# Kernel optimization log

Measured on AMD Instinct MI355X. Metric: run time of the kernel, lower is better.

The kernel has to match this reference:

```python
import jax, jax.numpy as jnp
import numpy as np
from jax import lax

N = 2048       # number of groups (rows of x)
T = 32768      # total tokens across all ragged segments
D_SEQ = 128    # per-token feature dim
D_LSTM = 512   # RNN hidden per direction (= min(512, d_hidden//2))
D_X = 512      # node feature dim (LazyLinear input)
D_HIDDEN = 2048
D_PROJ = D_HIDDEN - 2 * D_LSTM  # 1024


def setup_inputs() -> dict:
    key = jax.random.key(0)
    ks = jax.random.split(key, 12)
    x = jax.random.normal(ks[0], (N, D_X), jnp.float32)
    seqs = jax.random.normal(ks[1], (T, D_SEQ), jnp.float32)
    # sorted group ids; concat arange(N) to guarantee every group is present
    extra = jax.random.randint(ks[2], (T - N,), 0, N)
    masks = jnp.sort(jnp.concatenate([jnp.arange(N), extra]))
    s = 1.0 / np.sqrt(D_LSTM)
    u = lambda k, shape: jax.random.uniform(k, shape, jnp.float32, -s, s)
    return {
        "x": x, "seqs": seqs, "masks": masks,
        "W_ih_f": u(ks[3], (D_LSTM, D_SEQ)), "W_hh_f": u(ks[4], (D_LSTM, D_LSTM)), "b_f": u(ks[5], (D_LSTM,)),
        "W_ih_b": u(ks[6], (D_LSTM, D_SEQ)), "W_hh_b": u(ks[7], (D_LSTM, D_LSTM)), "b_b": u(ks[8], (D_LSTM,)),
        "Wx": u(ks[9], (D_PROJ, D_X)), "bx": u(ks[10], (D_PROJ,)),
    }


def _dir_scan(pre, starts, W_hh):
    # pre: [T, H] precomputed input projection (+bias); starts: [T] bool segment-start flags.
    # h_t = tanh(pre_t + W_hh h_{t-1}), with h reset to 0 at each segment start.
    def step(h, inp):
        p, st = inp
        h = jnp.tanh(p + jnp.where(st, 0.0, 1.0) * (h @ W_hh.T))
        return h, h
    h0 = jnp.zeros((pre.shape[1],), pre.dtype)
    _, hs = lax.scan(step, h0, (pre, starts))
    return hs  # [T, H]


def reference(x, seqs, masks, W_ih_f, W_hh_f, b_f, W_ih_b, W_hh_b, b_b, Wx, bx):
    # segment boundaries (masks is sorted -> contiguous segments)
    starts = jnp.concatenate([jnp.ones((1,), bool), masks[1:] != masks[:-1]])
    m_rev = masks[::-1]
    starts_rev = jnp.concatenate([jnp.ones((1,), bool), m_rev[1:] != m_rev[:-1]])

    # bidirectional tanh-RNN over each segment (single-layer, like nn.RNN)
    h_f = _dir_scan(seqs @ W_ih_f.T + b_f, starts, W_hh_f)                 # [T, 512]
    h_b = _dir_scan((seqs @ W_ih_b.T + b_b)[::-1], starts_rev, W_hh_b)[::-1]  # [T, 512]
    hidden = jnp.concatenate([h_f, h_b], axis=-1)                           # [T, 1024]

    # mean pool per segment -> one embedding per group
    counts = jax.ops.segment_sum(jnp.ones((masks.shape[0],), hidden.dtype), masks, num_segments=N)
    pooled = jax.ops.segment_sum(hidden, masks, num_segments=N) / counts[:, None]  # [N, 1024]

    # x projection then concat: [x_proj | pooled]
    return jnp.concatenate([x @ Wx.T + bx, pooled], axis=-1)  # [N, 2048]
```

## Files before the change

### kernel.cpp

```cpp
#include <hip/hip_runtime.h>
#include <cstdint>
#include <cstddef>

#define T_N    32768
#define N_SEG  2048
#define DSEQ   128
#define DLSTM  512
#define DX     512
#define DPROJ  1024
#define OUTW   2048
#define WSCALE 2873.6827f
#define SXQ    15.875f
#define LOG2E2 2.8853900817779268f
#define DEQH   (2.8853900817779268f/(2873.6827f*127.0f))
#define MAGICF 12582912.0f
#define MAGIC_C (12582912.0f + 127.0f)

typedef __attribute__((ext_vector_type(8))) short short8;
typedef __attribute__((ext_vector_type(4))) float f32x4;
typedef __attribute__((ext_vector_type(4))) int i32x4;

#if __has_builtin(__builtin_amdgcn_exp2f)
#define EXP2F(x) __builtin_amdgcn_exp2f(x)
#else
#define EXP2F(x) __expf((x) * 0.6931471805599453f)
#endif
#if __has_builtin(__builtin_amdgcn_rcpf)
#define RCPF(x) __builtin_amdgcn_rcpf(x)
#else
#define RCPF(x) (1.0f / (x))
#endif

#define PIN(x) asm volatile("" : "+v"(x))

__device__ inline unsigned int cvtpk(float a, float b) {
  unsigned int r;
  asm("v_cvt_pk_bf16_f32 %0, %1, %2" : "=v"(r) : "v"(a), "v"(b));
  return r;
}

__device__ inline unsigned pack4(unsigned b0, unsigned b1, unsigned b2, unsigned b3) {
#if __has_builtin(__builtin_amdgcn_perm)
  unsigned lo = __builtin_amdgcn_perm(b1, b0, 0x00000400u);
  unsigned hi = __builtin_amdgcn_perm(b3, b2, 0x00000400u);
  return __builtin_amdgcn_perm(hi, lo, 0x05040100u);
#else
  return (b0 & 255u) | ((b1 & 255u) << 8) | ((b2 & 255u) << 16) | (b3 << 24);
#endif
}

__global__ __launch_bounds__(256) void prep_kernel(
    const int* __restrict__ masks,
    const float* __restrict__ Whh_f, const float* __restrict__ Whh_b,
    const float* __restrict__ Wih_f, const float* __restrict__ Wih_b,
    signed char* __restrict__ W8, signed char* __restrict__ WX8,
    int* __restrict__ seg_start, int* __restrict__ seg_end,
    int* __restrict__ tile_ctr) {
  const int bid = blockIdx.x, tid = threadIdx.x;
  if (bid == 0 && tid == 0) *tile_ctr = 0;
  if (bid < 128) {
    int t = bid * 256 + tid;
    int m = masks[t];
    if (t == 0 || masks[t - 1] != m) seg_start[m] = t;
    if (t == T_N - 1 || masks[t + 1] != m) seg_end[m] = t + 1;
  } else if (bid < 256) {
    int id = (bid - 128) * 256 + tid;
    int lane = id & 63;
    int kt = (id >> 6) & 7;
    int mt = (id >> 9) & 3;
    int wv = (id >> 11) & 7;
    int dir = id >> 14;
    int rr = lane & 15;
    int n = wv * 64 + (rr >> 2) * 16 + mt * 4 + (rr & 3);
    int k0 = kt * 64 + (lane >> 4) * 16;
    const float* wp = (dir ? Whh_b : Whh_f) + (size_t)n * DLSTM + k0;
    signed char pkt[16];
#pragma unroll
    for (int q = 0; q < 4; ++q) {
      float4 v = *(const float4*)(wp + q * 4);
      float vv[4] = {v.x, v.y, v.z, v.w};
#pragma unroll
      for (int j = 0; j < 4; ++j) {
        int qq = (int)rintf(vv[j] * WSCALE);
        qq = qq > 127 ? 127 : (qq < -127 ? -127 : qq);
        pkt[q * 4 + j] = (signed char)qq;
      }
    }
    i32x4 v16;
    __builtin_memcpy(&v16, pkt, 16);
    *(i32x4*)&W8[(size_t)id * 16] = v16;
  } else {
    int id = (bid - 256) * 256 + tid;
    int lane = id & 63;
    int kt = (id >> 6) & 1;
    int mt = (id >> 7) & 3;
    int wv = (id >> 9) & 7;
    int dir = id >> 12;
    int rr = lane & 15;
    int n = wv * 64 + (rr >> 2) * 16 + mt * 4 + (rr & 3);
    int k0 = kt * 64 + (lane >> 4) * 16;
    const float* wp = (dir ? Wih_b : Wih_f) + (size_t)n * DSEQ + k0;
    signed char pkt[16];
#pragma unroll
    for (int q = 0; q < 4; ++q) {
      float4 v = *(const float4*)(wp + q * 4);
      float vv[4] = {v.x, v.y, v.z, v.w};
#pragma unroll
      for (int j = 0; j < 4; ++j) {
        int qq = (int)rintf(vv[j] * WSCALE);
        qq = qq > 127 ? 127 : (qq < -127 ? -127 : qq);
        pkt[q * 4 + j] = (signed char)qq;
      }
    }
    i32x4 v16;
    __builtin_memcpy(&v16, pkt, 16);
    *(i32x4*)&WX8[(size_t)id * 16] = v16;
  }
}

__global__ __launch_bounds__(512, 2) void fused_kernel(
    const float* __restrict__ seqs,
    const signed char* __restrict__ W8, const signed char* __restrict__ WX8,
    const int* __restrict__ seg_start, const int* __restrict__ seg_end,
    const float* __restrict__ b_f, const float* __restrict__ b_b,
    const float* __restrict__ x, const float* __restrict__ Wx,
    const float* __restrict__ bx, float* __restrict__ out,
    int* __restrict__ tile_ctr) {
  __shared__ __align__(16) char smem[36880];
  const int bid = blockIdx.x, tid = threadIdx.x;
  const int wv = tid >> 6, lane = tid & 63;

  {
    const int dir = bid & 1, bb = bid >> 1;
    const int chain = lane & 15, kgrp = lane >> 4;
    const int dbase = wv << 6;
    signed char* H = (signed char*)smem;
    signed char* Xs = (signed char*)(smem + 16896);
    int* meta = (int*)(smem + 21504);

    if (tid < 16) {
      int st = seg_start[bb * 16 + tid];
      meta[tid] = st;
      meta[16 + tid] = seg_end[bb * 16 + tid] - st;
    }
    {
      int r = tid >> 5, o = (tid & 31) << 4;
      *(i32x4*)(H + r * 528 + o) = (i32x4){0, 0, 0, 0};
    }

    i32x4 w[4][8], wx[4][2];
    {
      const signed char* wb = W8 + ((size_t)((dir << 3) + wv) << 15) + (lane << 4);
#pragma unroll
      for (int mt = 0; mt < 4; ++mt)
#pragma unroll
        for (int kt = 0; kt < 8; ++kt)
          w[mt][kt] = *(const i32x4*)(wb + (mt * 8 + kt) * 1024);
      const signed char* wxb = WX8 + ((size_t)((dir << 3) + wv) << 13) + (lane << 4);
#pragma unroll
      for (int mt = 0; mt < 4; ++mt)
#pragma unroll
        for (int kt = 0; kt < 2; ++kt)
          wx[mt][kt] = *(const i32x4*)(wxb + (mt * 2 + kt) * 1024);
    }
#pragma unroll
    for (int mt = 0; mt < 4; ++mt) {
#pragma unroll
      for (int kt = 0; kt < 8; ++kt) PIN(w[mt][kt]);
      PIN(wx[mt][0]); PIN(wx[mt][1]);
    }

    float bsc[16];
    {
      const float* bp = (dir ? b_b : b_f) + dbase + (kgrp << 4);
#pragma unroll
      for (int mt = 0; mt < 4; ++mt) {
        float4 u = *(const float4*)(bp + mt * 4);
        bsc[mt * 4 + 0] = u.x * LOG2E2; bsc[mt * 4 + 1] = u.y * LOG2E2;
        bsc[mt * 4 + 2] = u.z * LOG2E2; bsc[mt * 4 + 3] = u.w * LOG2E2;
      }
    }
    __syncthreads();

    int maxlen = 0;
#pragma unroll
    for (int c = 0; c < 16; ++c) {
      int l = meta[16 + c];
      maxlen = maxlen > l ? maxlen : l;
    }
    const int myLen = meta[16 + chain];
    const int csn = (wv << 1) + (lane >> 5);
    const int stStart = meta[csn], stLen = meta[16 + csn];
    const int jx = (lane & 31) << 2;

    {
      int t0 = dir ? (stStart + stLen - 1) : stStart;
      float4 xv0 = *(const float4*)(seqs + (size_t)t0 * DSEQ + jx);
      unsigned c0 = __float_as_uint(fminf(fmaxf(xv0.x * SXQ, -127.f), 127.f) + MAGICF);
      unsigned c1 = __float_as_uint(fminf(fmaxf(xv0.y * SXQ, -127.f), 127.f) + MAGICF);
      unsigned c2 = __float_as_uint(fminf(fmaxf(xv0.z * SXQ, -127.f), 127.f) + MAGICF);
      unsigned c3 = __float_as_uint(fminf(fmaxf(xv0.w * SXQ, -127.f), 127.f) + MAGICF);
      *(unsigned*)(Xs + csn * 144 + jx) = pack4(c0, c1, c2, c3);
    }
    __syncthreads();

    float pool[4][4];
#pragma unroll
    for (int mt = 0; mt < 4; ++mt)
#pragma unroll
      for (int r = 0; r < 4; ++r) pool[mt][r] = 0.f;

    int cur = 0;
    for (int s = 0; s < maxlen; ++s) {
      int sn = (s + 1 < stLen) ? (s + 1) : (stLen - 1);
      int tn = dir ? (stStart + stLen - 1 - sn) : (stStart + sn);
      float4 xv = *(const float4*)(seqs + (size_t)tn * DSEQ + jx);

      i32x4 acc[4], ax[4];
#pragma unroll
      for (int mt = 0; mt < 4; ++mt) {
        acc[mt] = (i32x4){0, 0, 0, 0};
        ax[mt] = (i32x4){0, 0, 0, 0};
      }
      {
        const signed char* xr = Xs + cur * 2304 + chain * 144;
#pragma unroll
        for (int kt = 0; kt < 2; ++kt) {
          i32x4 xb = *(const i32x4*)(xr + kt * 64 + (kgrp << 4));
#pragma unroll
          for (int mt = 0; mt < 4; ++mt)
            ax[mt] = __builtin_amdgcn_mfma_i32_16x16x64_i8(wx[mt][kt], xb, ax[mt], 0, 0, 0);
        }
        const signed char* hr = H + cur * 8448 + chain * 528;
#pragma unroll
        for (int kt = 0; kt < 8; ++kt) {
          i32x4 hb = *(const i32x4*)(hr + kt * 64 + (kgrp << 4));
#pragma unroll
          for (int mt = 0; mt < 4; ++mt)
            acc[mt] = __builtin_amdgcn_mfma_i32_16x16x64_i8(w[mt][kt], hb, acc[mt], 0, 0, 0);
        }
      }

      const float msk = (s < myLen) ? 1.f : 0.f;
      unsigned hw[4];
#pragma unroll
      for (int mt = 0; mt < 4; ++mt) {
        unsigned b[4];
#pragma unroll
        for (int r = 0; r < 4; ++r) {
          int comb = acc[mt][r] + (ax[mt][r] << 3);
          float x2 = fmaf((float)comb, DEQH, bsc[mt * 4 + r]);
          float e = EXP2F(x2);
          float rc = RCPF(e + 1.f);
          pool[mt][r] = fmaf(rc, msk, pool[mt][r]);
          b[r] = __float_as_uint(fmaf(-254.f, rc, MAGIC_C));
        }
        hw[mt] = pack4(b[0], b[1], b[2], b[3]);
      }
      *(uint4*)(H + (cur ^ 1) * 8448 + chain * 528 + dbase + (kgrp << 4)) =
          make_uint4(hw[0], hw[1], hw[2], hw[3]);
      {
        unsigned c0 = __float_as_uint(fminf(fmaxf(xv.x * SXQ, -127.f), 127.f) + MAGICF);
        unsigned c1 = __float_as_uint(fminf(fmaxf(xv.y * SXQ, -127.f), 127.f) + MAGICF);
        unsigned c2 = __float_as_uint(fminf(fmaxf(xv.z * SXQ, -127.f), 127.f) + MAGICF);
        unsigned c3 = __float_as_uint(fminf(fmaxf(xv.w * SXQ, -127.f), 127.f) + MAGICF);
        *(unsigned*)(Xs + (cur ^ 1) * 2304 + csn * 144 + jx) = pack4(c0, c1, c2, c3);
      }
      asm volatile("s_waitcnt lgkmcnt(0)" ::: "memory");
      __builtin_amdgcn_s_barrier();
      __builtin_amdgcn_sched_barrier(0);
      cur ^= 1;
    }

    const int sid = bb * 16 + chain;
    const float s2 = -2.0f / (float)myLen;
    float* op = out + (size_t)sid * OUTW + DPROJ + dir * DLSTM + dbase + (kgrp << 4);
#pragma unroll
    for (int mt = 0; mt < 4; ++mt)
      *(float4*)(op + mt * 4) =
          make_float4(fmaf(s2, pool[mt][0], 1.f), fmaf(s2, pool[mt][1], 1.f),
                      fmaf(s2, pool[mt][2], 1.f), fmaf(s2, pool[mt][3], 1.f));
  }

  {
    int* tileslot = (int*)(smem + 36864);
    unsigned short (*As)[72] = (unsigned short(*)[72])smem;
    unsigned short (*Bs)[72] = (unsigned short(*)[72])(smem + 18432);
    const int rowA = lane & 15, kgrp = lane >> 4;
    const int wm = (wv & 1) << 6, wn = (wv >> 1) << 5;
    const int srow = tid >> 2, skc = (tid & 3) << 3;

    for (;;) {
      __syncthreads();
      if (tid == 0) *tileslot = atomicAdd(tile_ctr, 1);
      __syncthreads();
      const int tile = *tileslot;
      if (tile >= 128) break;
      const int m0 = (tile >> 3) << 7, n0 = (tile & 7) << 7;

      f32x4 acc[4][2];
#pragma unroll
      for (int i = 0; i < 4; ++i)
#pragma unroll
        for (int j = 0; j < 2; ++j) acc[i][j] = (f32x4){0.f, 0.f, 0.f, 0.f};

      for (int k0 = 0; k0 < DX; k0 += 32) {
        __syncthreads();
        {
          const float* ap = x + (size_t)(m0 + srow) * DX + k0 + skc;
          float4 va0 = *(const float4*)ap;
          float4 va1 = *(const float4*)(ap + 4);
          unsigned wa[4] = {cvtpk(va0.x, va0.y), cvtpk(va0.z, va0.w),
                            cvtpk(va1.x, va1.y), cvtpk(va1.z, va1.w)};
          *(uint4*)&As[srow][skc] = *(uint4*)wa;
          const float* bp = Wx + (size_t)(n0 + srow) * DX + k0 + skc;
          float4 vb0 = *(const float4*)bp;
          float4 vb1 = *(const float4*)(bp + 4);
          unsigned wb2[4] = {cvtpk(vb0.x, vb0.y), cvtpk(vb0.z, vb0.w),
                             cvtpk(vb1.x, vb1.y), cvtpk(vb1.z, vb1.w)};
          *(uint4*)&Bs[srow][skc] = *(uint4*)wb2;
        }
        __syncthreads();
        short8 af[4], bf[2];
#pragma unroll
        for (int mt = 0; mt < 4; ++mt)
          af[mt] = *(const short8*)&As[wm + mt * 16 + rowA][kgrp << 3];
#pragma unroll
        for (int nt = 0; nt < 2; ++nt)
          bf[nt] = *(const short8*)&Bs[wn + nt * 16 + rowA][kgrp << 3];
#pragma unroll
        for (int mt = 0; mt < 4; ++mt)
#pragma unroll
          for (int nt = 0; nt < 2; ++nt)
            acc[mt][nt] = __builtin_amdgcn_mfma_f32_16x16x32_bf16(af[mt], bf[nt], acc[mt][nt], 0, 0, 0);
      }

#pragma unroll
      for (int mt = 0; mt < 4; ++mt)
#pragma unroll
        for (int nt = 0; nt < 2; ++nt) {
          int n = n0 + wn + nt * 16 + rowA;
          float bv = bx[n];
#pragma unroll
          for (int r = 0; r < 4; ++r) {
            int m = m0 + wm + mt * 16 + (kgrp << 2) + r;
            out[(size_t)m * OUTW + n] = acc[mt][nt][r] + bv;
          }
        }
    }
  }
}

extern "C" void kernel_launch(void* const* d_in, const int* in_sizes, int n_in,
                              void* d_out, int out_size, void* d_ws, size_t ws_size,
                              hipStream_t stream) {
  const float* x     = (const float*)d_in[0];
  const float* seqs  = (const float*)d_in[1];
  const int*   masks = (const int*)d_in[2];
  const float* Wih_f = (const float*)d_in[3];
  const float* Whh_f = (const float*)d_in[4];
  const float* b_f   = (const float*)d_in[5];
  const float* Wih_b = (const float*)d_in[6];
  const float* Whh_b = (const float*)d_in[7];
  const float* b_b   = (const float*)d_in[8];
  const float* Wx    = (const float*)d_in[9];
  const float* bx    = (const float*)d_in[10];
  float* out = (float*)d_out;

  char* ws = (char*)d_ws;
  signed char* W8  = (signed char*)ws;
  signed char* WX8 = (signed char*)(ws + (size_t)512 * 1024);
  int* seg_start = (int*)(ws + (size_t)640 * 1024);
  int* seg_end   = seg_start + N_SEG;
  int* tile_ctr  = seg_end + N_SEG;

  prep_kernel<<<288, 256, 0, stream>>>(masks, Whh_f, Whh_b, Wih_f, Wih_b,
                                       W8, WX8, seg_start, seg_end, tile_ctr);
  fused_kernel<<<256, 512, 0, stream>>>(seqs, W8, WX8, seg_start, seg_end,
                                        b_f, b_b, x, Wx, bx, out, tile_ctr);
}
```

Baseline: 65.07 us.

## Sort segments by length so each RNN block groups similar-length chains

A new single-block kernel counting-sorts the segments by length, longest first, and writes permuted segment ids, starts and lengths. Each fused-kernel block now runs 16 chains of similar length, so it no longer steps to a much longer maxlen than most of its chains need. Finished blocks can then move on sooner to the work-stolen projection GEMM tiles. The backward direction walks the sorted order in reverse, so long forward blocks pair with short backward blocks. The cost is an extra serial kernel launch and an indirect output row index.

```diff
diff --git a/kernel.cpp b/kernel.cpp
--- a/kernel.cpp
+++ b/kernel.cpp
@@ -118,10 +118,49 @@
   }
 }
 
+__global__ __launch_bounds__(1024) void csort_kernel(
+    const int* __restrict__ seg_start, const int* __restrict__ seg_end,
+    int* __restrict__ s_sid, int* __restrict__ s_st, int* __restrict__ s_ln) {
+  __shared__ int A_[2048];
+  __shared__ int B_[2048];
+  const int tid = threadIdx.x;
+  for (int i = tid; i < 2048; i += 1024) A_[i] = 0;
+  __syncthreads();
+  for (int i = tid; i < N_SEG; i += 1024) {
+    int len = seg_end[i] - seg_start[i];
+    atomicAdd(&A_[len < 2047 ? len : 2047], 1);
+  }
+  __syncthreads();
+  int* src = A_;
+  int* dst = B_;
+  for (int d = 1; d < 2048; d <<= 1) {
+    for (int i = tid; i < 2048; i += 1024) {
+      int v = src[i];
+      if (i + d < 2048) v += src[i + d];
+      dst[i] = v;
+    }
+    __syncthreads();
+    int* tp = src; src = dst; dst = tp;
+  }
+  for (int i = tid; i < 2048; i += 1024)
+    dst[i] = (i + 1 < 2048) ? src[i + 1] : 0;
+  __syncthreads();
+  for (int i = tid; i < N_SEG; i += 1024) {
+    int st = seg_start[i];
+    int len = seg_end[i] - st;
+    int b = len < 2047 ? len : 2047;
+    int pos = atomicAdd(&dst[b], 1);
+    s_sid[pos] = i;
+    s_st[pos] = st;
+    s_ln[pos] = len;
+  }
+}
+
 __global__ __launch_bounds__(512, 2) void fused_kernel(
     const float* __restrict__ seqs,
     const signed char* __restrict__ W8, const signed char* __restrict__ WX8,
-    const int* __restrict__ seg_start, const int* __restrict__ seg_end,
+    const int* __restrict__ s_sid_g, const int* __restrict__ s_st_g,
+    const int* __restrict__ s_ln_g,
     const float* __restrict__ b_f, const float* __restrict__ b_b,
     const float* __restrict__ x, const float* __restrict__ Wx,
     const float* __restrict__ bx, float* __restrict__ out,
@@ -131,7 +170,9 @@
   const int wv = tid >> 6, lane = tid & 63;
 
   {
-    const int dir = bid & 1, bb = bid >> 1;
+    const int dir = bid & 1;
+    const int idx = bid >> 1;
+    const int bb = dir ? (127 - idx) : idx;
     const int chain = lane & 15, kgrp = lane >> 4;
     const int dbase = wv << 6;
     signed char* H = (signed char*)smem;
@@ -139,9 +180,9 @@
     int* meta = (int*)(smem + 21504);
 
     if (tid < 16) {
-      int st = seg_start[bb * 16 + tid];
-      meta[tid] = st;
-      meta[16 + tid] = seg_end[bb * 16 + tid] - st;
+      meta[tid] = s_sid_g[bb * 16 + tid];
+      meta[16 + tid] = s_st_g[bb * 16 + tid];
+      meta[32 + tid] = s_ln_g[bb * 16 + tid];
     }
     {
       int r = tid >> 5, o = (tid & 31) << 4;
@@ -182,15 +223,10 @@
     }
     __syncthreads();
 
-    int maxlen = 0;
-#pragma unroll
-    for (int c = 0; c < 16; ++c) {
-      int l = meta[16 + c];
-      maxlen = maxlen > l ? maxlen : l;
-    }
-    const int myLen = meta[16 + chain];
+    const int maxlen = meta[32];
+    const int myLen = meta[32 + chain];
     const int csn = (wv << 1) + (lane >> 5);
-    const int stStart = meta[csn], stLen = meta[16 + csn];
+    const int stStart = meta[16 + csn], stLen = meta[32 + csn];
     const int jx = (lane & 31) << 2;
 
     {
@@ -272,7 +308,7 @@
       cur ^= 1;
     }
 
-    const int sid = bb * 16 + chain;
+    const int sid = meta[chain];
     const float s2 = -2.0f / (float)myLen;
     float* op = out + (size_t)sid * OUTW + DPROJ + dir * DLSTM + dbase + (kgrp << 4);
 #pragma unroll
@@ -373,9 +409,13 @@
   int* seg_start = (int*)(ws + (size_t)640 * 1024);
   int* seg_end   = seg_start + N_SEG;
   int* tile_ctr  = seg_end + N_SEG;
+  int* s_sid     = tile_ctr + 64;
+  int* s_st      = s_sid + N_SEG;
+  int* s_ln      = s_st + N_SEG;
 
   prep_kernel<<<288, 256, 0, stream>>>(masks, Whh_f, Whh_b, Wih_f, Wih_b,
                                        W8, WX8, seg_start, seg_end, tile_ctr);
-  fused_kernel<<<256, 512, 0, stream>>>(seqs, W8, WX8, seg_start, seg_end,
+  csort_kernel<<<1, 1024, 0, stream>>>(seg_start, seg_end, s_sid, s_st, s_ln);
+  fused_kernel<<<256, 512, 0, stream>>>(seqs, W8, WX8, s_sid, s_st, s_ln,
                                         b_f, b_b, x, Wx, bx, out, tile_ctr);
 }
```

After: 68.82 us. 5.8% more time.

## Split RNN hidden dimension across 16 waves with 1024-thread blocks

Applied to the files above, without the earlier changes.

Doubles the block size to 1024 threads, so each wave owns 32 hidden units (2 MFMA row tiles) instead of 64. The int8 weight prepack layout, bias loading, H/X staging writes, pooling output and the bf16 projection GEMM tiling are all remapped to the 16-wave split. The goal is to shorten the per-step serial critical path of the recurrence by halving MFMA work per wave and spreading it over more SIMDs. In exchange, each step's barrier now synchronizes 16 waves, and the staging stores become smaller.

```diff
diff --git a/kernel.cpp b/kernel.cpp
--- a/kernel.cpp
+++ b/kernel.cpp
@@ -67,11 +67,10 @@
     int id = (bid - 128) * 256 + tid;
     int lane = id & 63;
     int kt = (id >> 6) & 7;
-    int mt = (id >> 9) & 3;
-    int wv = (id >> 11) & 7;
+    int mt = (id >> 9) & 1;
+    int wv = (id >> 10) & 15;
     int dir = id >> 14;
-    int rr = lane & 15;
-    int n = wv * 64 + (rr >> 2) * 16 + mt * 4 + (rr & 3);
+    int n = wv * 32 + mt * 16 + (lane & 15);
     int k0 = kt * 64 + (lane >> 4) * 16;
     const float* wp = (dir ? Whh_b : Whh_f) + (size_t)n * DLSTM + k0;
     signed char pkt[16];
@@ -93,11 +92,10 @@
     int id = (bid - 256) * 256 + tid;
     int lane = id & 63;
     int kt = (id >> 6) & 1;
-    int mt = (id >> 7) & 3;
-    int wv = (id >> 9) & 7;
+    int mt = (id >> 7) & 1;
+    int wv = (id >> 8) & 15;
     int dir = id >> 12;
-    int rr = lane & 15;
-    int n = wv * 64 + (rr >> 2) * 16 + mt * 4 + (rr & 3);
+    int n = wv * 32 + mt * 16 + (lane & 15);
     int k0 = kt * 64 + (lane >> 4) * 16;
     const float* wp = (dir ? Wih_b : Wih_f) + (size_t)n * DSEQ + k0;
     signed char pkt[16];
@@ -118,7 +116,7 @@
   }
 }
 
-__global__ __launch_bounds__(512, 2) void fused_kernel(
+__global__ __launch_bounds__(1024, 4) void fused_kernel(
     const float* __restrict__ seqs,
     const signed char* __restrict__ W8, const signed char* __restrict__ WX8,
     const int* __restrict__ seg_start, const int* __restrict__ seg_end,
@@ -133,7 +131,7 @@
   {
     const int dir = bid & 1, bb = bid >> 1;
     const int chain = lane & 15, kgrp = lane >> 4;
-    const int dbase = wv << 6;
+    const int dbase = wv << 5;
     signed char* H = (signed char*)smem;
     signed char* Xs = (signed char*)(smem + 16896);
     int* meta = (int*)(smem + 21504);
@@ -144,40 +142,40 @@
       meta[16 + tid] = seg_end[bb * 16 + tid] - st;
     }
     {
-      int r = tid >> 5, o = (tid & 31) << 4;
-      *(i32x4*)(H + r * 528 + o) = (i32x4){0, 0, 0, 0};
-    }
-
-    i32x4 w[4][8], wx[4][2];
+      int r = tid >> 6, o = lane << 3;
+      *(uint2*)(H + r * 528 + o) = make_uint2(0u, 0u);
+    }
+
+    i32x4 w[2][8], wx[2][2];
     {
-      const signed char* wb = W8 + ((size_t)((dir << 3) + wv) << 15) + (lane << 4);
-#pragma unroll
-      for (int mt = 0; mt < 4; ++mt)
+      const signed char* wb = W8 + ((size_t)((dir << 4) + wv) << 14) + (lane << 4);
+#pragma unroll
+      for (int mt = 0; mt < 2; ++mt)
 #pragma unroll
         for (int kt = 0; kt < 8; ++kt)
           w[mt][kt] = *(const i32x4*)(wb + (mt * 8 + kt) * 1024);
-      const signed char* wxb = WX8 + ((size_t)((dir << 3) + wv) << 13) + (lane << 4);
-#pragma unroll
-      for (int mt = 0; mt < 4; ++mt)
+      const signed char* wxb = WX8 + ((size_t)((dir << 4) + wv) << 12) + (lane << 4);
+#pragma unroll
+      for (int mt = 0; mt < 2; ++mt)
 #pragma unroll
         for (int kt = 0; kt < 2; ++kt)
           wx[mt][kt] = *(const i32x4*)(wxb + (mt * 2 + kt) * 1024);
     }
 #pragma unroll
-    for (int mt = 0; mt < 4; ++mt) {
+    for (int mt = 0; mt < 2; ++mt) {
 #pragma unroll
       for (int kt = 0; kt < 8; ++kt) PIN(w[mt][kt]);
       PIN(wx[mt][0]); PIN(wx[mt][1]);
     }
 
-    float bsc[16];
+    float bsc[2][4];
     {
-      const float* bp = (dir ? b_b : b_f) + dbase + (kgrp << 4);
-#pragma unroll
-      for (int mt = 0; mt < 4; ++mt) {
-        float4 u = *(const float4*)(bp + mt * 4);
-        bsc[mt * 4 + 0] = u.x * LOG2E2; bsc[mt * 4 + 1] = u.y * LOG2E2;
-        bsc[mt * 4 + 2] = u.z * LOG2E2; bsc[mt * 4 + 3] = u.w * LOG2E2;
+      const float* bsrc = dir ? b_b : b_f;
+#pragma unroll
+      for (int mt = 0; mt < 2; ++mt) {
+        float4 u = *(const float4*)(bsrc + dbase + mt * 16 + (kgrp << 2));
+        bsc[mt][0] = u.x * LOG2E2; bsc[mt][1] = u.y * LOG2E2;
+        bsc[mt][2] = u.z * LOG2E2; bsc[mt][3] = u.w * LOG2E2;
       }
     }
     __syncthreads();
@@ -189,24 +187,22 @@
       maxlen = maxlen > l ? maxlen : l;
     }
     const int myLen = meta[16 + chain];
-    const int csn = (wv << 1) + (lane >> 5);
-    const int stStart = meta[csn], stLen = meta[16 + csn];
-    const int jx = (lane & 31) << 2;
+    const int stStart = meta[wv], stLen = meta[16 + wv];
+    const int jx = lane << 1;
 
     {
       int t0 = dir ? (stStart + stLen - 1) : stStart;
-      float4 xv0 = *(const float4*)(seqs + (size_t)t0 * DSEQ + jx);
+      float2 xv0 = *(const float2*)(seqs + (size_t)t0 * DSEQ + jx);
       unsigned c0 = __float_as_uint(fminf(fmaxf(xv0.x * SXQ, -127.f), 127.f) + MAGICF);
       unsigned c1 = __float_as_uint(fminf(fmaxf(xv0.y * SXQ, -127.f), 127.f) + MAGICF);
-      unsigned c2 = __float_as_uint(fminf(fmaxf(xv0.z * SXQ, -127.f), 127.f) + MAGICF);
-      unsigned c3 = __float_as_uint(fminf(fmaxf(xv0.w * SXQ, -127.f), 127.f) + MAGICF);
-      *(unsigned*)(Xs + csn * 144 + jx) = pack4(c0, c1, c2, c3);
+      *(unsigned short*)(Xs + wv * 144 + jx) =
+          (unsigned short)((c0 & 255u) | ((c1 & 255u) << 8));
     }
     __syncthreads();
 
-    float pool[4][4];
-#pragma unroll
-    for (int mt = 0; mt < 4; ++mt)
+    float pool[2][4];
+#pragma unroll
+    for (int mt = 0; mt < 2; ++mt)
 #pragma unroll
       for (int r = 0; r < 4; ++r) pool[mt][r] = 0.f;
 
@@ -214,11 +210,11 @@
     for (int s = 0; s < maxlen; ++s) {
       int sn = (s + 1 < stLen) ? (s + 1) : (stLen - 1);
       int tn = dir ? (stStart + stLen - 1 - sn) : (stStart + sn);
-      float4 xv = *(const float4*)(seqs + (size_t)tn * DSEQ + jx);
-
-      i32x4 acc[4], ax[4];
-#pragma unroll
-      for (int mt = 0; mt < 4; ++mt) {
+      float2 xv = *(const float2*)(seqs + (size_t)tn * DSEQ + jx);
+
+      i32x4 acc[2], ax[2];
+#pragma unroll
+      for (int mt = 0; mt < 2; ++mt) {
         acc[mt] = (i32x4){0, 0, 0, 0};
         ax[mt] = (i32x4){0, 0, 0, 0};
       }
@@ -228,7 +224,7 @@
         for (int kt = 0; kt < 2; ++kt) {
           i32x4 xb = *(const i32x4*)(xr + kt * 64 + (kgrp << 4));
 #pragma unroll
-          for (int mt = 0; mt < 4; ++mt)
+          for (int mt = 0; mt < 2; ++mt)
             ax[mt] = __builtin_amdgcn_mfma_i32_16x16x64_i8(wx[mt][kt], xb, ax[mt], 0, 0, 0);
         }
         const signed char* hr = H + cur * 8448 + chain * 528;
@@ -236,35 +232,32 @@
         for (int kt = 0; kt < 8; ++kt) {
           i32x4 hb = *(const i32x4*)(hr + kt * 64 + (kgrp << 4));
 #pragma unroll
-          for (int mt = 0; mt < 4; ++mt)
+          for (int mt = 0; mt < 2; ++mt)
             acc[mt] = __builtin_amdgcn_mfma_i32_16x16x64_i8(w[mt][kt], hb, acc[mt], 0, 0, 0);
         }
       }
 
       const float msk = (s < myLen) ? 1.f : 0.f;
-      unsigned hw[4];
-#pragma unroll
-      for (int mt = 0; mt < 4; ++mt) {
+#pragma unroll
+      for (int mt = 0; mt < 2; ++mt) {
         unsigned b[4];
 #pragma unroll
         for (int r = 0; r < 4; ++r) {
           int comb = acc[mt][r] + (ax[mt][r] << 3);
-          float x2 = fmaf((float)comb, DEQH, bsc[mt * 4 + r]);
+          float x2 = fmaf((float)comb, DEQH, bsc[mt][r]);
           float e = EXP2F(x2);
           float rc = RCPF(e + 1.f);
           pool[mt][r] = fmaf(rc, msk, pool[mt][r]);
           b[r] = __float_as_uint(fmaf(-254.f, rc, MAGIC_C));
         }
-        hw[mt] = pack4(b[0], b[1], b[2], b[3]);
-      }
-      *(uint4*)(H + (cur ^ 1) * 8448 + chain * 528 + dbase + (kgrp << 4)) =
-          make_uint4(hw[0], hw[1], hw[2], hw[3]);
+        *(unsigned*)(H + (cur ^ 1) * 8448 + chain * 528 + dbase + mt * 16 + (kgrp << 2)) =
+            pack4(b[0], b[1], b[2], b[3]);
+      }
       {
         unsigned c0 = __float_as_uint(fminf(fmaxf(xv.x * SXQ, -127.f), 127.f) + MAGICF);
         unsigned c1 = __float_as_uint(fminf(fmaxf(xv.y * SXQ, -127.f), 127.f) + MAGICF);
-        unsigned c2 = __float_as_uint(fminf(fmaxf(xv.z * SXQ, -127.f), 127.f) + MAGICF);
-        unsigned c3 = __float_as_uint(fminf(fmaxf(xv.w * SXQ, -127.f), 127.f) + MAGICF);
-        *(unsigned*)(Xs + (cur ^ 1) * 2304 + csn * 144 + jx) = pack4(c0, c1, c2, c3);
+        *(unsigned short*)(Xs + (cur ^ 1) * 2304 + wv * 144 + jx) =
+            (unsigned short)((c0 & 255u) | ((c1 & 255u) << 8));
       }
       asm volatile("s_waitcnt lgkmcnt(0)" ::: "memory");
       __builtin_amdgcn_s_barrier();
@@ -274,10 +267,10 @@
 
     const int sid = bb * 16 + chain;
     const float s2 = -2.0f / (float)myLen;
-    float* op = out + (size_t)sid * OUTW + DPROJ + dir * DLSTM + dbase + (kgrp << 4);
-#pragma unroll
-    for (int mt = 0; mt < 4; ++mt)
-      *(float4*)(op + mt * 4) =
+    float* op = out + (size_t)sid * OUTW + DPROJ + dir * DLSTM + dbase + (kgrp << 2);
+#pragma unroll
+    for (int mt = 0; mt < 2; ++mt)
+      *(float4*)(op + mt * 16) =
           make_float4(fmaf(s2, pool[mt][0], 1.f), fmaf(s2, pool[mt][1], 1.f),
                       fmaf(s2, pool[mt][2], 1.f), fmaf(s2, pool[mt][3], 1.f));
   }
@@ -287,8 +280,8 @@
     unsigned short (*As)[72] = (unsigned short(*)[72])smem;
     unsigned short (*Bs)[72] = (unsigned short(*)[72])(smem + 18432);
     const int rowA = lane & 15, kgrp = lane >> 4;
-    const int wm = (wv & 1) << 6, wn = (wv >> 1) << 5;
-    const int srow = tid >> 2, skc = (tid & 3) << 3;
+    const int wm = (wv >> 2) << 5, wn = (wv & 3) << 5;
+    const int srow = tid >> 3, skc = (tid & 7) << 2;
 
     for (;;) {
       __syncthreads();
@@ -298,45 +291,39 @@
       if (tile >= 128) break;
       const int m0 = (tile >> 3) << 7, n0 = (tile & 7) << 7;
 
-      f32x4 acc[4][2];
-#pragma unroll
-      for (int i = 0; i < 4; ++i)
+      f32x4 acc[2][2];
+#pragma unroll
+      for (int i = 0; i < 2; ++i)
 #pragma unroll
         for (int j = 0; j < 2; ++j) acc[i][j] = (f32x4){0.f, 0.f, 0.f, 0.f};
 
       for (int k0 = 0; k0 < DX; k0 += 32) {
         __syncthreads();
         {
-          const float* ap = x + (size_t)(m0 + srow) * DX + k0 + skc;
-          float4 va0 = *(const float4*)ap;
-          float4 va1 = *(const float4*)(ap + 4);
-          unsigned wa[4] = {cvtpk(va0.x, va0.y), cvtpk(va0.z, va0.w),
-                            cvtpk(va1.x, va1.y), cvtpk(va1.z, va1.w)};
-          *(uint4*)&As[srow][skc] = *(uint4*)wa;
-          const float* bp = Wx + (size_t)(n0 + srow) * DX + k0 + skc;
-          float4 vb0 = *(const float4*)bp;
-          float4 vb1 = *(const float4*)(bp + 4);
-          unsigned wb2[4] = {cvtpk(vb0.x, vb0.y), cvtpk(vb0.z, vb0.w),
-                             cvtpk(vb1.x, vb1.y), cvtpk(vb1.z, vb1.w)};
-          *(uint4*)&Bs[srow][skc] = *(uint4*)wb2;
+          float4 va = *(const float4*)(x + (size_t)(m0 + srow) * DX + k0 + skc);
+          unsigned wa[2] = {cvtpk(va.x, va.y), cvtpk(va.z, va.w)};
+          *(uint2*)&As[srow][skc] = *(uint2*)wa;
+          float4 vb = *(const float4*)(Wx + (size_t)(n0 + srow) * DX + k0 + skc);
+          unsigned wb2[2] = {cvtpk(vb.x, vb.y), cvtpk(vb.z, vb.w)};
+          *(uint2*)&Bs[srow][skc] = *(uint2*)wb2;
         }
         __syncthreads();
-        short8 af[4], bf[2];
-#pragma unroll
-        for (int mt = 0; mt < 4; ++mt)
+        short8 af[2], bf[2];
+#pragma unroll
+        for (int mt = 0; mt < 2; ++mt)
           af[mt] = *(const short8*)&As[wm + mt * 16 + rowA][kgrp << 3];
 #pragma unroll
         for (int nt = 0; nt < 2; ++nt)
           bf[nt] = *(const short8*)&Bs[wn + nt * 16 + rowA][kgrp << 3];
 #pragma unroll
-        for (int mt = 0; mt < 4; ++mt)
+        for (int mt = 0; mt < 2; ++mt)
 #pragma unroll
           for (int nt = 0; nt < 2; ++nt)
             acc[mt][nt] = __builtin_amdgcn_mfma_f32_16x16x32_bf16(af[mt], bf[nt], acc[mt][nt], 0, 0, 0);
       }
 
 #pragma unroll
-      for (int mt = 0; mt < 4; ++mt)
+      for (int mt = 0; mt < 2; ++mt)
 #pragma unroll
         for (int nt = 0; nt < 2; ++nt) {
           int n = n0 + wn + nt * 16 + rowA;
@@ -376,6 +363,6 @@
 
   prep_kernel<<<288, 256, 0, stream>>>(masks, Whh_f, Whh_b, Wih_f, Wih_b,
                                        W8, WX8, seg_start, seg_end, tile_ctr);
-  fused_kernel<<<256, 512, 0, stream>>>(seqs, W8, WX8, seg_start, seg_end,
-                                        b_f, b_b, x, Wx, bx, out, tile_ctr);
-}
+  fused_kernel<<<256, 1024, 0, stream>>>(seqs, W8, WX8, seg_start, seg_end,
+                                         b_f, b_b, x, Wx, bx, out, tile_ctr);
+}
```

After: 75.64 us. 1.16x slower.
